# Performance work log

Measured on AMD Instinct MI355X. Metric: run time of the kernel, lower is better.

Reference implementation:

```python
import jax, jax.numpy as jnp
import numpy as np

NUM_HEADS = 16
BUDGET = 1024


def layer_norm(x, g, b, eps=1e-5):
    mu = jnp.mean(x, axis=-1, keepdims=True)
    var = jnp.mean((x - mu) ** 2, axis=-1, keepdims=True)
    return (x - mu) / jnp.sqrt(var + eps) * g + b


def setup_inputs() -> dict:
    key = jax.random.key(0)
    ks = jax.random.split(key, 6)
    B, N, D = 2, 2048, 1024
    H, Dh = NUM_HEADS, 1024 // NUM_HEADS
    sc = 1.0 / np.sqrt(D).astype(np.float32)
    X = jax.random.normal(ks[0], (B, N, D), jnp.float32)
    W_q = jax.random.normal(ks[1], (D, D), jnp.float32) * sc
    W_k = jax.random.normal(ks[2], (D, D), jnp.float32) * sc
    W_v = jax.random.normal(ks[3], (D, D), jnp.float32) * sc
    W_o = jax.random.normal(ks[4], (D, D), jnp.float32) * sc
    return dict(
        X=X, W_q=W_q, W_k=W_k, W_v=W_v, W_o=W_o,
        gamma_q=jnp.ones((D,), jnp.float32), beta_q=jnp.zeros((D,), jnp.float32),
        gamma_k=jnp.ones((D,), jnp.float32), beta_k=jnp.zeros((D,), jnp.float32),
        cache_k=jnp.zeros((B, H, BUDGET, Dh), jnp.float32),
        cache_v=jnp.zeros((B, H, BUDGET, Dh), jnp.float32),
        start_pos=0,
    )


def reference(X, W_q, W_k, W_v, W_o, gamma_q, beta_q, gamma_k, beta_k,
              cache_k, cache_v, start_pos):
    B, N, D = X.shape
    H = NUM_HEADS
    Dh = D // H
    budget = cache_k.shape[2]
    M = start_pos + N  # total kv length

    XQ = layer_norm(X @ W_q, gamma_q, beta_q).reshape(B, N, H, Dh).transpose(0, 2, 1, 3)
    XK = layer_norm(X @ W_k, gamma_k, beta_k).reshape(B, N, H, Dh).transpose(0, 2, 1, 3)
    XV = (X @ W_v).reshape(B, N, H, Dh).transpose(0, 2, 1, 3)

    K = jnp.concatenate([cache_k[:B, :, :start_pos], XK], axis=2)  # (B,H,M,Dh)
    V = jnp.concatenate([cache_v[:B, :, :start_pos], XV], axis=2)

    logits = jnp.einsum('bhnd,bhmd->bhnm', XQ, K) / np.float32(np.sqrt(Dh))
    n_idx = jnp.arange(N)[:, None]
    m_idx = jnp.arange(M)[None, :]
    causal_keep = (m_idx < start_pos) | ((m_idx - start_pos) <= n_idx)  # (N,M)
    logits = jnp.where(causal_keep, logits, -jnp.inf)

    # --- selection (eviction) scores from head 0 ---
    S = jax.nn.relu(logits[:, 0])                        # (B,N,M); relu(-inf)=0
    S = S.at[:, :, start_pos].set(0.0)                   # never evict <BOS>-like slot
    S = S.at[:, :, start_pos:].multiply(1.0 - jnp.eye(N, dtype=S.dtype))  # zero diagonal
    S = jnp.roll(S, 1, axis=1).at[:, 0, :].set(0.0)      # shift: scores apply from next query
    Fm = jnp.cumsum(S, axis=1)                           # (B,N,M) cumulative eviction scores

    # --- sequential heavy-hitter eviction ---
    unmasked0 = jnp.broadcast_to(jnp.arange(budget, dtype=jnp.int32), (B, budget))
    kpos = jnp.arange(budget, dtype=jnp.int32)[None, :]

    def step(unmasked, i):
        new_idx = jnp.concatenate(
            [unmasked, jnp.full((B, 1), i, unmasked.dtype)], axis=1)     # (B,budget+1)
        row = jax.lax.dynamic_index_in_dim(Fm, i - start_pos, axis=1, keepdims=False)  # (B,M)
        scores = jnp.take_along_axis(row, new_idx, axis=1)
        idx = jnp.argmax(scores, axis=-1)                                # (B,)
        evicted = jnp.take_along_axis(new_idx, idx[:, None], axis=1)[:, 0]
        unmasked = jnp.where(kpos < idx[:, None], new_idx[:, :budget], new_idx[:, 1:])
        return unmasked, evicted

    steps = jnp.arange(max(budget, start_pos), M, dtype=jnp.int32)       # (T,)
    _, evicts = jax.lax.scan(step, unmasked0, steps)                     # evicts (T,B)

    big = jnp.int32(M + start_pos + 1)
    evict_time = jnp.full((B, M), big, jnp.int32)
    evict_time = evict_time.at[jnp.arange(B, dtype=jnp.int32)[None, :], evicts].min(steps[:, None])
    # query row j is pruned from key m iff (j + start_pos) >= evict_time[m]
    prune_keep = (jnp.arange(N)[:, None] + start_pos) < evict_time[:, None, :]  # (B,N,M)

    logits = jnp.where(prune_keep[:, None], logits, -jnp.inf)
    attn = jax.nn.softmax(logits, axis=-1)
    O = jnp.einsum('bhnm,bhmd->bhnd', attn, V).transpose(0, 2, 1, 3).reshape(B, N, D)
    return O @ W_o
```

## Files before the change

kernel.cpp:

```cpp
#include <hip/hip_runtime.h>

#define B_    2
#define N_    2048
#define D_    1024
#define H_    16
#define DH_   64
#define M_    2048
#define ROWS_ 4096
#define BUD_  1024

typedef unsigned short u16;
typedef unsigned int   u32;
typedef unsigned long long u64;
typedef __attribute__((ext_vector_type(8))) short short8;
typedef __attribute__((ext_vector_type(4))) float floatx4;

__device__ __forceinline__ u16 f2b(float f) {
    u32 u = __float_as_uint(f);
    return (u16)((u + 0x7FFFu + ((u >> 16) & 1u)) >> 16);
}
__device__ __forceinline__ float b2f(u16 h) {
    return __uint_as_float(((u32)h) << 16);
}

__global__ __launch_bounds__(256) void cast_x_kernel(
    const float* __restrict__ X, u16* __restrict__ Xhi, u16* __restrict__ Xlo)
{
    int idx = (blockIdx.x * 256 + threadIdx.x) * 4;
    float4 v = *(const float4*)&X[idx];
    u16 h0 = f2b(v.x), h1 = f2b(v.y), h2 = f2b(v.z), h3 = f2b(v.w);
    ushort4 hv; hv.x = h0; hv.y = h1; hv.z = h2; hv.w = h3;
    *(ushort4*)&Xhi[idx] = hv;
    ushort4 lv;
    lv.x = f2b(v.x - b2f(h0)); lv.y = f2b(v.y - b2f(h1));
    lv.z = f2b(v.z - b2f(h2)); lv.w = f2b(v.w - b2f(h3));
    *(ushort4*)&Xlo[idx] = lv;
}

__global__ __launch_bounds__(1024) void cast_w_kernel(
    const float* __restrict__ W, u16* __restrict__ Whi, u16* __restrict__ Wlo,
    int do_lo)
{
    __shared__ float tile[32][33];
    int tx = threadIdx.x, ty = threadIdx.y;
    int x = blockIdx.x * 32 + tx, y = blockIdx.y * 32 + ty;
    tile[ty][tx] = W[(size_t)y * D_ + x];
    __syncthreads();
    float v = tile[tx][ty];
    int n = blockIdx.x * 32 + ty, k = blockIdx.y * 32 + tx;
    u16 h = f2b(v);
    Whi[(size_t)n * D_ + k] = h;
    if (do_lo) Wlo[(size_t)n * D_ + k] = f2b(v - b2f(h));
}

__global__ __launch_bounds__(256) void gemm_kernel(
    const u16* __restrict__ Ah, const u16* __restrict__ Al,
    const u16* __restrict__ Bh, const u16* __restrict__ Bl,
    int mode, float* __restrict__ C)
{
    __shared__ __align__(16) u16 sAh[128 * 32];
    __shared__ __align__(16) u16 sBh[128 * 32];
    __shared__ __align__(16) u16 sAl[128 * 32];
    __shared__ __align__(16) u16 sBl[128 * 32];
    int tid = threadIdx.x;
    int lane = tid & 63, wv = tid >> 6;
    int wr = wv >> 1, wc = wv & 1;
    int quad = lane >> 4, l16 = lane & 15;
    int m0 = blockIdx.y * 128, n0 = blockIdx.x * 128;

    floatx4 acc[4][4];
    floatx4 zero = {0.f, 0.f, 0.f, 0.f};
#pragma unroll
    for (int i = 0; i < 4; ++i)
#pragma unroll
        for (int j = 0; j < 4; ++j) acc[i][j] = zero;

    for (int k0 = 0; k0 < 1024; k0 += 32) {
#pragma unroll
        for (int it = 0; it < 2; ++it) {
            int e = (tid + it * 256) * 8;
            int r = e >> 5, c = e & 31;
            *(uint4*)&sAh[e] = *(const uint4*)&Ah[(size_t)(m0 + r) * 1024 + k0 + c];
            *(uint4*)&sBh[e] = *(const uint4*)&Bh[(size_t)(n0 + r) * 1024 + k0 + c];
            if (mode) {
                *(uint4*)&sAl[e] = *(const uint4*)&Al[(size_t)(m0 + r) * 1024 + k0 + c];
                *(uint4*)&sBl[e] = *(const uint4*)&Bl[(size_t)(n0 + r) * 1024 + k0 + c];
            }
        }
        __syncthreads();
        short8 ah[4], al[4], bh[4], bl[4];
#pragma unroll
        for (int x = 0; x < 4; ++x) {
            int ra = (wr * 64 + x * 16 + l16) * 32 + quad * 8;
            int rb = (wc * 64 + x * 16 + l16) * 32 + quad * 8;
            ah[x] = *(const short8*)&sAh[ra];
            bh[x] = *(const short8*)&sBh[rb];
            if (mode) {
                al[x] = *(const short8*)&sAl[ra];
                bl[x] = *(const short8*)&sBl[rb];
            }
        }
#pragma unroll
        for (int mi = 0; mi < 4; ++mi)
#pragma unroll
            for (int ni = 0; ni < 4; ++ni) {
                acc[mi][ni] = __builtin_amdgcn_mfma_f32_16x16x32_bf16(
                    ah[mi], bh[ni], acc[mi][ni], 0, 0, 0);
                if (mode) {
                    acc[mi][ni] = __builtin_amdgcn_mfma_f32_16x16x32_bf16(
                        ah[mi], bl[ni], acc[mi][ni], 0, 0, 0);
                    acc[mi][ni] = __builtin_amdgcn_mfma_f32_16x16x32_bf16(
                        al[mi], bh[ni], acc[mi][ni], 0, 0, 0);
                }
            }
        __syncthreads();
    }
#pragma unroll
    for (int mi = 0; mi < 4; ++mi)
#pragma unroll
        for (int ni = 0; ni < 4; ++ni)
#pragma unroll
            for (int r = 0; r < 4; ++r) {
                int row = m0 + wr * 64 + mi * 16 + quad * 4 + r;
                int col = n0 + wc * 64 + ni * 16 + l16;
                C[(size_t)row * 1024 + col] = acc[mi][ni][r];
            }
}

__global__ __launch_bounds__(256) void lnpack_kernel(
    const float* __restrict__ Y, const float* __restrict__ gamma,
    const float* __restrict__ beta, u16* __restrict__ Pk,
    float* __restrict__ head0, int do_ln)
{
    int r = blockIdx.x;
    int tid = threadIdx.x;
    float4 v = *(const float4*)&Y[(size_t)r * D_ + tid * 4];
    float mu = 0.f, rsig = 1.f;
    __shared__ float sS[4], sQ[4];
    if (do_ln) {
        float s = v.x + v.y + v.z + v.w;
        float q = v.x * v.x + v.y * v.y + v.z * v.z + v.w * v.w;
#pragma unroll
        for (int d = 1; d < 64; d <<= 1) { s += __shfl_xor(s, d); q += __shfl_xor(q, d); }
        if ((tid & 63) == 0) { sS[tid >> 6] = s; sQ[tid >> 6] = q; }
        __syncthreads();
        s = sS[0] + sS[1] + sS[2] + sS[3];
        q = sQ[0] + sQ[1] + sQ[2] + sQ[3];
        mu = s * (1.f / 1024.f);
        float var = q * (1.f / 1024.f) - mu * mu;
        rsig = rsqrtf(var + 1e-5f);
    }
    int b = r >> 11, n = r & 2047;
    float xs[4] = {v.x, v.y, v.z, v.w};
#pragma unroll
    for (int j = 0; j < 4; ++j) {
        int c = tid * 4 + j;
        float val = do_ln ? ((xs[j] - mu) * rsig * gamma[c] + beta[c]) : xs[j];
        int h = c >> 6, dh = c & 63;
        Pk[(((size_t)b * H_ + h) * N_ + n) * DH_ + dh] = f2b(val);
        if (head0 && c < 64) head0[(size_t)r * 64 + c] = val;
    }
}

__global__ void s_kernel(const float* __restrict__ q0,
                         const float* __restrict__ k0, float* __restrict__ S)
{
    int b = blockIdx.z;
    int n0 = blockIdx.y * 16, m0 = blockIdx.x * 16;
    int tx = threadIdx.x, ty = threadIdx.y;
    int n = n0 + ty, m = m0 + tx;
    float* out = S + ((size_t)b * N_ + n) * M_ + m;
    if (m0 > n0 + 15) { *out = 0.f; return; }
    __shared__ float sq[16][65], sk[16][65];
    int tid = ty * 16 + tx;
    {
        int rr = tid >> 4, cc = (tid & 15) * 4;
        float4 qa = *(const float4*)&q0[((size_t)b * N_ + n0 + rr) * 64 + cc];
        sq[rr][cc] = qa.x; sq[rr][cc + 1] = qa.y; sq[rr][cc + 2] = qa.z; sq[rr][cc + 3] = qa.w;
        float4 ka = *(const float4*)&k0[((size_t)b * N_ + m0 + rr) * 64 + cc];
        sk[rr][cc] = ka.x; sk[rr][cc + 1] = ka.y; sk[rr][cc + 2] = ka.z; sk[rr][cc + 3] = ka.w;
    }
    __syncthreads();
    float acc = 0.f;
#pragma unroll 8
    for (int d = 0; d < 64; ++d) acc += sq[ty][d] * sk[tx][d];
    float val;
    if (m < n && m != 0) val = fmaxf(acc * 0.125f, 0.f); else val = 0.f;
    *out = val;
}

__global__ __launch_bounds__(256) void p_kernel(const float* __restrict__ S,
                                                float* __restrict__ P)
{
    int b = blockIdx.z, c = blockIdx.y;
    int m = blockIdx.x * 256 + threadIdx.x;
    const float* base = S + ((size_t)b * N_ + c * 128) * M_ + m;
    float s = 0.f;
    for (int j = 0; j < 128; ++j) s += base[(size_t)j * M_];
    P[((size_t)b * 8 + c) * M_ + m] = s;
}


__device__ __forceinline__ void vsel(float& va, u32& la, float vb, u32 lb) {
    bool tk = vb > va;
    va = tk ? vb : va;
    la = tk ? lb : la;
}

template<int CTRL, int RMASK>
__device__ __forceinline__ void dpp_max_pack(float& v, u32& lo) {
    int hi = __float_as_int(v);
    int hi_o = __builtin_amdgcn_update_dpp(hi, hi, CTRL, RMASK, 0xF, false);
    int lo_o = __builtin_amdgcn_update_dpp((int)lo, (int)lo, CTRL, RMASK, 0xF, false);
    long long a = (long long)((((u64)(u32)hi) << 32) | lo);
    long long b = (long long)((((u64)(u32)hi_o) << 32) | (u32)lo_o);
    bool tk = b > a;
    v = tk ? __int_as_float(hi_o) : v;
    lo = tk ? (u32)lo_o : lo;
}

__device__ __forceinline__ void wave_argmax_to63(float& v, u32& lo) {
    dpp_max_pack<0x121, 0xF>(v, lo);
    dpp_max_pack<0x122, 0xF>(v, lo);
    dpp_max_pack<0x124, 0xF>(v, lo);
    dpp_max_pack<0x128, 0xF>(v, lo);
    dpp_max_pack<0x142, 0xA>(v, lo);
    dpp_max_pack<0x143, 0xC>(v, lo);
}

#define GLOAD(dst, voff, ptr, imm)                                    \
    asm volatile("global_load_dwordx4 %0, %1, %2 offset:" #imm        \
                 : "=v"(dst) : "v"(voff), "s"(ptr) : "memory")

#define ISSUE2(bank, row)                                             \
    {                                                                 \
        u32 r_ = (u32)((row) < 2047 ? (row) : 2047);                  \
        u32 vo = wbyte + r_ * 8192u;                                  \
        GLOAD(bank[0], vo, Sb, 0);                                    \
        GLOAD(bank[1], vo, Sb, 1024);                                 \
    }

#define VWAIT6()                                                      \
    do { asm volatile("s_waitcnt vmcnt(6)" ::: "memory");             \
         __builtin_amdgcn_sched_barrier(0); } while (0)
#define VWAIT0()                                                      \
    do { asm volatile("s_waitcnt vmcnt(0)" ::: "memory");             \
         __builtin_amdgcn_sched_barrier(0); } while (0)

__device__ __forceinline__ void evict_step4(
    int i, int t, int w, int par,
    const u32 (&lov)[2][4], float (&cum)[2][4], int (&evti)[2][4],
    const floatx4 (&bank)[2], uint2 (*spair)[4])
{
    const float NEGINF = __uint_as_float(0xFF800000u);
    float v0 = cum[0][0]; u32 l0 = lov[0][0];
    vsel(v0, l0, cum[0][1], lov[0][1]);
    float v1 = cum[0][2]; u32 l1 = lov[0][2];
    vsel(v1, l1, cum[0][3], lov[0][3]);
    vsel(v0, l0, v1, l1);
    float v2 = cum[1][0]; u32 l2 = lov[1][0];
    vsel(v2, l2, cum[1][1], lov[1][1]);
    float v3 = cum[1][2]; u32 l3 = lov[1][2];
    vsel(v3, l3, cum[1][3], lov[1][3]);
    vsel(v2, l2, v3, l3);
    vsel(v0, l0, v2, l2);
    wave_argmax_to63(v0, l0);
    if (t == 63) spair[par][w] = make_uint2(l0, (u32)__float_as_int(v0));
    asm volatile("s_waitcnt lgkmcnt(0)" ::: "memory");
    __builtin_amdgcn_sched_barrier(0);
    __builtin_amdgcn_s_barrier();
    __builtin_amdgcn_sched_barrier(0);
    uint2 q0 = spair[par][0], q1 = spair[par][1];
    uint2 q2 = spair[par][2], q3 = spair[par][3];
    long long k0 = (long long)((((u64)q0.y) << 32) | q0.x);
    long long k1 = (long long)((((u64)q1.y) << 32) | q1.x);
    long long k2 = (long long)((((u64)q2.y) << 32) | q2.x);
    long long k3 = (long long)((((u64)q3.y) << 32) | q3.x);
    long long ba = k0 > k1 ? k0 : k1;
    long long bb = k2 > k3 ? k2 : k3;
    long long bst = ba > bb ? ba : bb;
    const u32 lostar = (u32)(bst & 0xFFFFFFFFll);
#pragma unroll
    for (int c = 0; c < 2; ++c) {
        cum[c][0] += bank[c][0]; cum[c][1] += bank[c][1];
        cum[c][2] += bank[c][2]; cum[c][3] += bank[c][3];
    }
#pragma unroll
    for (int c = 0; c < 2; ++c)
#pragma unroll
        for (int e = 0; e < 4; ++e) {
            bool hit = (lov[c][e] == lostar);
            cum[c][e] = hit ? NEGINF : cum[c][e];
            evti[c][e] = hit ? i : evti[c][e];
        }
}

__global__ __launch_bounds__(256) void evict_kernel(
    const float* __restrict__ S, const float* __restrict__ P,
    int* __restrict__ evt)
{
    int b = blockIdx.x;
    int tid = threadIdx.x;
    int w = tid >> 6, t = tid & 63;
    const float* Sb = S + (size_t)b * N_ * M_;
    int* evtb = evt + b * M_;
    const int mbase = 512 * w + 4 * t;
    const u32 wbyte = (u32)(2048 * w + 16 * t);
    __shared__ uint2 spair[2][4];
    u32 lov[2][4];
    int evti[2][4];
#pragma unroll
    for (int c = 0; c < 2; ++c)
#pragma unroll
        for (int e = 0; e < 4; ++e) {
            lov[c][e] = (u32)(2048 - (mbase + 256 * c + e));
            evti[c][e] = 0x3FFFFFFF;
        }
    float cum[2][4];
#pragma unroll
    for (int c = 0; c < 2; ++c) {
        float ax = 0.f, ay = 0.f, az = 0.f, aw = 0.f;
#pragma unroll
        for (int cc = 0; cc < 8; ++cc) {
            floatx4 pv = *(const floatx4*)&P[((size_t)b * 8 + cc) * M_ + mbase + 256 * c];
            ax += pv[0]; ay += pv[1]; az += pv[2]; aw += pv[3];
        }
        cum[c][0] = ax; cum[c][1] = ay; cum[c][2] = az; cum[c][3] = aw;
    }
    VWAIT0();
    floatx4 bA[2], bB[2], bC[2], bD[2];
    ISSUE2(bA, 1024)
    ISSUE2(bB, 1025)
    ISSUE2(bC, 1026)
    ISSUE2(bD, 1027)
#pragma unroll 1
    for (int ip = 1024; ip < 2048; ip += 4) {
        VWAIT6();
        evict_step4(ip + 0, t, w, 0, lov, cum, evti, bA, spair);
        ISSUE2(bA, ip + 4)
        VWAIT6();
        evict_step4(ip + 1, t, w, 1, lov, cum, evti, bB, spair);
        ISSUE2(bB, ip + 5)
        VWAIT6();
        evict_step4(ip + 2, t, w, 0, lov, cum, evti, bC, spair);
        ISSUE2(bC, ip + 6)
        VWAIT6();
        evict_step4(ip + 3, t, w, 1, lov, cum, evti, bD, spair);
        ISSUE2(bD, ip + 7)
    }
    VWAIT0();
#pragma unroll
    for (int c = 0; c < 2; ++c) {
        int4 o; o.x = evti[c][0]; o.y = evti[c][1];
        o.z = evti[c][2]; o.w = evti[c][3];
        *(int4*)&evtb[mbase + 256 * c] = o;
    }
}

__global__ __launch_bounds__(256) void flash_kernel(
    const u16* __restrict__ Qb, const u16* __restrict__ Kb,
    const u16* __restrict__ Vb, const int* __restrict__ evt,
    u16* __restrict__ Ob)
{
    int bh = blockIdx.y;
    int b = bh >> 4, h = bh & 15;
    int q0 = blockIdx.x * 64;
    int tid = threadIdx.x, lane = tid & 63, w = tid >> 6;
    int quad = lane >> 4, l16 = lane & 15;
    const u16* Qh = Qb + (size_t)bh * N_ * DH_;
    const u16* Kh = Kb + (size_t)bh * N_ * DH_;
    const u16* Vh = Vb + (size_t)bh * N_ * DH_;
    __shared__ __align__(16) u16 sK[64 * 64];
    __shared__ __align__(16) u16 sV[64 * 64];
    __shared__ __align__(16) u16 sP[4][16 * 64];
    __shared__ int sevt[64];

    short8 aq0 = *(const short8*)&Qh[(size_t)(q0 + w * 16 + l16) * 64 + quad * 8];
    short8 aq1 = *(const short8*)&Qh[(size_t)(q0 + w * 16 + l16) * 64 + quad * 8 + 32];

    floatx4 zero = {0.f, 0.f, 0.f, 0.f};
    floatx4 accO[4];
#pragma unroll
    for (int d = 0; d < 4; ++d) accO[d] = zero;
    float m_i[4] = {-1e30f, -1e30f, -1e30f, -1e30f};
    float l_i[4] = {0.f, 0.f, 0.f, 0.f};

    int ktiles = blockIdx.x + 1;
    for (int kt = 0; kt < ktiles; ++kt) {
        int k0 = kt * 64;
#pragma unroll
        for (int it = 0; it < 2; ++it) {
            int e = (tid + it * 256) * 8;
            int r = e >> 6, c = e & 63;
            *(uint4*)&sK[e] = *(const uint4*)&Kh[(size_t)(k0 + r) * 64 + c];
            uint4 vv = *(const uint4*)&Vh[(size_t)(k0 + r) * 64 + c];
            sV[(c + 0) * 64 + r] = (u16)(vv.x & 0xFFFF);
            sV[(c + 1) * 64 + r] = (u16)(vv.x >> 16);
            sV[(c + 2) * 64 + r] = (u16)(vv.y & 0xFFFF);
            sV[(c + 3) * 64 + r] = (u16)(vv.y >> 16);
            sV[(c + 4) * 64 + r] = (u16)(vv.z & 0xFFFF);
            sV[(c + 5) * 64 + r] = (u16)(vv.z >> 16);
            sV[(c + 6) * 64 + r] = (u16)(vv.w & 0xFFFF);
            sV[(c + 7) * 64 + r] = (u16)(vv.w >> 16);
        }
        if (tid < 64) sevt[tid] = evt[b * M_ + k0 + tid];
        __syncthreads();

        floatx4 lg[4];
        int nbase = q0 + w * 16 + quad * 4;
#pragma unroll
        for (int s = 0; s < 4; ++s) {
            floatx4 sc = zero;
            short8 bk0 = *(const short8*)&sK[(s * 16 + l16) * 64 + quad * 8];
            short8 bk1 = *(const short8*)&sK[(s * 16 + l16) * 64 + quad * 8 + 32];
            sc = __builtin_amdgcn_mfma_f32_16x16x32_bf16(aq0, bk0, sc, 0, 0, 0);
            sc = __builtin_amdgcn_mfma_f32_16x16x32_bf16(aq1, bk1, sc, 0, 0, 0);
            int m = k0 + s * 16 + l16;
            int ev = sevt[s * 16 + l16];
#pragma unroll
            for (int r = 0; r < 4; ++r) {
                int n = nbase + r;
                bool keep = (m <= n) && (n < ev);
                lg[s][r] = keep ? sc[r] * 0.125f : -1e30f;
            }
        }
        float mnew[4], scale[4], rs[4];
#pragma unroll
        for (int r = 0; r < 4; ++r) {
            float mx = fmaxf(fmaxf(lg[0][r], lg[1][r]), fmaxf(lg[2][r], lg[3][r]));
#pragma unroll
            for (int d = 1; d < 16; d <<= 1) mx = fmaxf(mx, __shfl_xor(mx, d));
            mnew[r] = fmaxf(m_i[r], mx);
            scale[r] = __expf(m_i[r] - mnew[r]);
            m_i[r] = mnew[r];
            rs[r] = 0.f;
        }
#pragma unroll
        for (int s = 0; s < 4; ++s)
#pragma unroll
            for (int r = 0; r < 4; ++r) {
                float p = __expf(lg[s][r] - mnew[r]);
                rs[r] += p;
                sP[w][(quad * 4 + r) * 64 + s * 16 + l16] = f2b(p);
            }
#pragma unroll
        for (int r = 0; r < 4; ++r) {
            float t_ = rs[r];
#pragma unroll
            for (int d = 1; d < 16; d <<= 1) t_ += __shfl_xor(t_, d);
            l_i[r] = l_i[r] * scale[r] + t_;
        }
#pragma unroll
        for (int dd = 0; dd < 4; ++dd) {
            accO[dd][0] *= scale[0]; accO[dd][1] *= scale[1];
            accO[dd][2] *= scale[2]; accO[dd][3] *= scale[3];
        }
        short8 ap0 = *(const short8*)&sP[w][l16 * 64 + quad * 8];
        short8 ap1 = *(const short8*)&sP[w][l16 * 64 + quad * 8 + 32];
#pragma unroll
        for (int dd = 0; dd < 4; ++dd) {
            short8 bv0 = *(const short8*)&sV[(dd * 16 + l16) * 64 + quad * 8];
            short8 bv1 = *(const short8*)&sV[(dd * 16 + l16) * 64 + quad * 8 + 32];
            accO[dd] = __builtin_amdgcn_mfma_f32_16x16x32_bf16(ap0, bv0, accO[dd], 0, 0, 0);
            accO[dd] = __builtin_amdgcn_mfma_f32_16x16x32_bf16(ap1, bv1, accO[dd], 0, 0, 0);
        }
        __syncthreads();
    }
#pragma unroll
    for (int dd = 0; dd < 4; ++dd)
#pragma unroll
        for (int r = 0; r < 4; ++r) {
            int n = q0 + w * 16 + quad * 4 + r;
            int col = h * 64 + dd * 16 + l16;
            Ob[((size_t)b * N_ + n) * D_ + col] = f2b(accO[dd][r] / l_i[r]);
        }
}

extern "C" void kernel_launch(void* const* d_in, const int* in_sizes, int n_in,
                              void* d_out, int out_size, void* d_ws, size_t ws_size,
                              hipStream_t stream)
{
    (void)in_sizes; (void)n_in; (void)out_size; (void)ws_size;
    const float* X  = (const float*)d_in[0];
    const float* Wq = (const float*)d_in[1];
    const float* Wk = (const float*)d_in[2];
    const float* Wv = (const float*)d_in[3];
    const float* Wo = (const float*)d_in[4];
    const float* gq = (const float*)d_in[5];
    const float* bq = (const float*)d_in[6];
    const float* gk = (const float*)d_in[7];
    const float* bk = (const float*)d_in[8];

    char* p = (char*)d_ws;
    const size_t SZ_XH = (size_t)ROWS_ * D_ * 2;
    const size_t SZ_W  = (size_t)D_ * D_ * 2;
    const size_t SZ_Y  = (size_t)ROWS_ * D_ * 4;
    const size_t SZ_PK = (size_t)ROWS_ * D_ * 2;
    const size_t SZ_H0 = (size_t)ROWS_ * 64 * 4;

    size_t o = 0;
    u16* Xhi = (u16*)(p + o); o += SZ_XH;
    u16* Xlo = (u16*)(p + o); o += SZ_XH;
    u16* Wqh = (u16*)(p + o); o += SZ_W;
    u16* Wql = (u16*)(p + o); o += SZ_W;
    u16* Wkh = (u16*)(p + o); o += SZ_W;
    u16* Wkl = (u16*)(p + o); o += SZ_W;
    u16* Wvh = (u16*)(p + o); o += SZ_W;
    u16* Woh = (u16*)(p + o); o += SZ_W;
    float* Yq = (float*)(p + o); size_t oYq = o; o += SZ_Y;
    float* Yk = (float*)(p + o); o += SZ_Y;
    float* Yv = (float*)(p + o); o += SZ_Y;
    u16* Qb = (u16*)(p + o); o += SZ_PK;
    u16* Kb = (u16*)(p + o); o += SZ_PK;
    u16* Vb = (u16*)(p + o); o += SZ_PK;
    float* q0s = (float*)(p + o); o += SZ_H0;
    float* k0s = (float*)(p + o); o += SZ_H0;
    float* Pp  = (float*)(p + o); o += (size_t)B_ * 8 * M_ * 4;
    int* evt   = (int*)(p + o);  o += (size_t)B_ * M_ * 4;
    float* S = (float*)(p + oYq);
    u16* Ob  = Xhi;

    cast_x_kernel<<<ROWS_ * D_ / (256 * 4), 256, 0, stream>>>(X, Xhi, Xlo);
    dim3 wgrid(32, 32), wblk(32, 32);
    cast_w_kernel<<<wgrid, wblk, 0, stream>>>(Wq, Wqh, Wql, 1);
    cast_w_kernel<<<wgrid, wblk, 0, stream>>>(Wk, Wkh, Wkl, 1);
    cast_w_kernel<<<wgrid, wblk, 0, stream>>>(Wv, Wvh, nullptr, 0);
    cast_w_kernel<<<wgrid, wblk, 0, stream>>>(Wo, Woh, nullptr, 0);

    dim3 ggrid(D_ / 128, ROWS_ / 128);
    gemm_kernel<<<ggrid, 256, 0, stream>>>(Xhi, Xlo, Wqh, Wql, 1, Yq);
    gemm_kernel<<<ggrid, 256, 0, stream>>>(Xhi, Xlo, Wkh, Wkl, 1, Yk);
    gemm_kernel<<<ggrid, 256, 0, stream>>>(Xhi, nullptr, Wvh, nullptr, 0, Yv);

    lnpack_kernel<<<ROWS_, 256, 0, stream>>>(Yq, gq, bq, Qb, q0s, 1);
    lnpack_kernel<<<ROWS_, 256, 0, stream>>>(Yk, gk, bk, Kb, k0s, 1);
    lnpack_kernel<<<ROWS_, 256, 0, stream>>>(Yv, nullptr, nullptr, Vb, nullptr, 0);

    s_kernel<<<dim3(M_ / 16, N_ / 16, B_), dim3(16, 16), 0, stream>>>(q0s, k0s, S);
    p_kernel<<<dim3(M_ / 256, 8, B_), 256, 0, stream>>>(S, Pp);
    evict_kernel<<<B_, 256, 0, stream>>>(S, Pp, evt);

    flash_kernel<<<dim3(N_ / 64, B_ * H_), 256, 0, stream>>>(Qb, Kb, Vb, evt, Ob);
    gemm_kernel<<<ggrid, 256, 0, stream>>>(Ob, nullptr, Woh, nullptr, 0, (float*)d_out);
}
```

Measured before the change: 916.9 us.

## Overlap eviction scan with flash attention for rows unaffected by eviction

Splits flash attention into two launches. Query tiles below the cache budget need no eviction mask, so they run in the same launch as the two-block eviction scan and use otherwise idle CUs. The remaining tiles run afterwards with the eviction times. This relies on early rows never being evicted and adds a branch on the mask pointer inside the flash code.

```diff
diff --git a/kernel.cpp b/kernel.cpp
--- a/kernel.cpp
+++ b/kernel.cpp
@@ -199,7 +199,6 @@
     for (int j = 0; j < 128; ++j) s += base[(size_t)j * M_];
     P[((size_t)b * 8 + c) * M_ + m] = s;
 }
-
 
 __device__ __forceinline__ void vsel(float& va, u32& la, float vb, u32 lb) {
     bool tk = vb > va;
@@ -295,9 +294,9 @@
         }
 }
 
-__global__ __launch_bounds__(256) void evict_kernel(
-    const float* __restrict__ S, const float* __restrict__ P,
-    int* __restrict__ evt)
+__device__ void evict_role(const float* __restrict__ S,
+                           const float* __restrict__ P,
+                           int* __restrict__ evt)
 {
     int b = blockIdx.x;
     int tid = threadIdx.x;
@@ -357,14 +356,12 @@
     }
 }
 
-__global__ __launch_bounds__(256) void flash_kernel(
+__device__ void flash_role(
     const u16* __restrict__ Qb, const u16* __restrict__ Kb,
-    const u16* __restrict__ Vb, const int* __restrict__ evt,
-    u16* __restrict__ Ob)
-{
-    int bh = blockIdx.y;
+    const u16* __restrict__ Vb, const int* __restrict__ evtg,
+    u16* __restrict__ Ob, int bh, int q0, int ktiles)
+{
     int b = bh >> 4, h = bh & 15;
-    int q0 = blockIdx.x * 64;
     int tid = threadIdx.x, lane = tid & 63, w = tid >> 6;
     int quad = lane >> 4, l16 = lane & 15;
     const u16* Qh = Qb + (size_t)bh * N_ * DH_;
@@ -385,7 +382,6 @@
     float m_i[4] = {-1e30f, -1e30f, -1e30f, -1e30f};
     float l_i[4] = {0.f, 0.f, 0.f, 0.f};
 
-    int ktiles = blockIdx.x + 1;
     for (int kt = 0; kt < ktiles; ++kt) {
         int k0 = kt * 64;
 #pragma unroll
@@ -403,7 +399,7 @@
             sV[(c + 6) * 64 + r] = (u16)(vv.w & 0xFFFF);
             sV[(c + 7) * 64 + r] = (u16)(vv.w >> 16);
         }
-        if (tid < 64) sevt[tid] = evt[b * M_ + k0 + tid];
+        if (evtg && tid < 64) sevt[tid] = evtg[b * M_ + k0 + tid];
         __syncthreads();
 
         floatx4 lg[4];
@@ -416,7 +412,7 @@
             sc = __builtin_amdgcn_mfma_f32_16x16x32_bf16(aq0, bk0, sc, 0, 0, 0);
             sc = __builtin_amdgcn_mfma_f32_16x16x32_bf16(aq1, bk1, sc, 0, 0, 0);
             int m = k0 + s * 16 + l16;
-            int ev = sevt[s * 16 + l16];
+            int ev = evtg ? sevt[s * 16 + l16] : 0x7FFFFFFF;
 #pragma unroll
             for (int r = 0; r < 4; ++r) {
                 int n = nbase + r;
@@ -474,6 +470,30 @@
             int col = h * 64 + dd * 16 + l16;
             Ob[((size_t)b * N_ + n) * D_ + col] = f2b(accO[dd][r] / l_i[r]);
         }
+}
+
+__global__ __launch_bounds__(256) void fused_evict_flash1(
+    const float* __restrict__ S, const float* __restrict__ P,
+    int* __restrict__ evt,
+    const u16* __restrict__ Qb, const u16* __restrict__ Kb,
+    const u16* __restrict__ Vb, u16* __restrict__ Ob)
+{
+    if (blockIdx.x < 2) {
+        evict_role(S, P, evt);
+    } else {
+        int fid = blockIdx.x - 2;
+        int bh = fid >> 4, j = fid & 15;
+        flash_role(Qb, Kb, Vb, nullptr, Ob, bh, j * 64, j + 1);
+    }
+}
+
+__global__ __launch_bounds__(256) void flash2_kernel(
+    const u16* __restrict__ Qb, const u16* __restrict__ Kb,
+    const u16* __restrict__ Vb, const int* __restrict__ evt,
+    u16* __restrict__ Ob)
+{
+    int j = blockIdx.x + 16;
+    flash_role(Qb, Kb, Vb, evt, Ob, blockIdx.y, j * 64, j + 1);
 }
 
 extern "C" void kernel_launch(void* const* d_in, const int* in_sizes, int n_in,
@@ -538,8 +558,9 @@
 
     s_kernel<<<dim3(M_ / 16, N_ / 16, B_), dim3(16, 16), 0, stream>>>(q0s, k0s, S);
     p_kernel<<<dim3(M_ / 256, 8, B_), 256, 0, stream>>>(S, Pp);
-    evict_kernel<<<B_, 256, 0, stream>>>(S, Pp, evt);
-
-    flash_kernel<<<dim3(N_ / 64, B_ * H_), 256, 0, stream>>>(Qb, Kb, Vb, evt, Ob);
+
+    fused_evict_flash1<<<514, 256, 0, stream>>>(S, Pp, evt, Qb, Kb, Vb, Ob);
+    flash2_kernel<<<dim3(16, B_ * H_), 256, 0, stream>>>(Qb, Kb, Vb, evt, Ob);
+
     gemm_kernel<<<ggrid, 256, 0, stream>>>(Ob, nullptr, Woh, nullptr, 0, (float*)d_out);
 }
```

New measurement: 844.6 us. 1.09x faster.
